# Performance work log

Measured on AMD Instinct MI355X. Metric: run time of the kernel, lower is better.

## Reference

```python
import jax, jax.numpy as jnp
import numpy as np

N = 100_000          # nodes
E = 600_000          # directed edges, stored in reverse pairs (2i <-> 2i+1)
D_NODE = 128
D_EDGE = 16
UNITS = 128
EDGE_STEPS = 4
NODE_STEPS = 4


def setup_inputs() -> dict:
    key = jax.random.key(0)
    ks = jax.random.split(key, 10)
    s = 0.05
    # undirected pairs -> both directions so every edge has a reverse edge
    u = jax.random.randint(ks[0], (E // 2,), 0, N, dtype=jnp.int32)
    v = jax.random.randint(ks[1], (E // 2,), 0, N, dtype=jnp.int32)
    edge_src = jnp.stack([u, v], axis=1).reshape(-1)  # [E]
    edge_dst = jnp.stack([v, u], axis=1).reshape(-1)  # [E]
    edge_rev = (jnp.arange(E, dtype=jnp.int32) ^ 1)   # reverse-edge index
    return dict(
        node_feature=jax.random.normal(ks[2], (N, D_NODE), jnp.float32),
        edge_feature=jax.random.normal(ks[3], (E, D_EDGE), jnp.float32),
        W_init=jax.random.normal(ks[4], (D_NODE + D_EDGE, UNITS), jnp.float32) * s,
        b_init=jnp.zeros((UNITS,), jnp.float32),
        W_edge=jax.random.normal(ks[5], (EDGE_STEPS, UNITS, UNITS), jnp.float32) * s,
        b_edge=jnp.zeros((EDGE_STEPS, UNITS), jnp.float32),
        W_gin0=jax.random.normal(ks[6], (D_NODE + UNITS, UNITS), jnp.float32) * s,
        W_gin=jax.random.normal(ks[7], (NODE_STEPS - 1, UNITS, UNITS), jnp.float32) * s,
        b_gin=jnp.zeros((NODE_STEPS, UNITS), jnp.float32),
        eps=jnp.zeros((NODE_STEPS,), jnp.float32),
        edge_src=edge_src,
        edge_dst=edge_dst,
        edge_rev=edge_rev,
    )


def reference(node_feature, edge_feature, W_init, b_init, W_edge, b_edge,
              W_gin0, W_gin, b_gin, eps, edge_src, edge_dst, edge_rev):
    relu = jax.nn.relu
    seg = lambda x: jax.ops.segment_sum(x, edge_dst, num_segments=N)

    # ---- EdgeConv stack (D-MPNN directed edge message passing) ----
    # initial edge state: act(W [x_src || e])
    h = relu(jnp.concatenate([node_feature[edge_src], edge_feature], axis=-1)
             @ W_init + b_init)                                  # [E, U]
    for t in range(EDGE_STEPS):
        agg = seg(h)                                             # [N, U] incoming sums
        m = agg[edge_src] - h[edge_rev]                          # exclude reverse edge
        h = relu(h + m @ W_edge[t] + b_edge[t])                  # residual edge update

    # ---- NodeReadout: sum incoming edge states per node ----
    readout = seg(h)                                             # [N, U]
    x = jnp.concatenate([node_feature, readout], axis=-1)        # [N, D_NODE + U]

    # ---- GINConv stack (use_edge_features=False) ----
    for t in range(NODE_STEPS):
        agg = seg(x[edge_src])                                   # [N, d] neighbor sum
        W = W_gin0 if t == 0 else W_gin[t - 1]
        x = relu(((1.0 + eps[t]) * x + agg) @ W + b_gin[t])      # [N, U]

    return x, h
```

## Files before the change

### kernel.cpp

```cpp
#include <hip/hip_runtime.h>

#define N_NODES 100000
#define N_EDGES 600000
#define SCAN_NB ((N_NODES + 255) / 256)

#define WOFF_I  0
#define WOFF_E  20480
#define WOFF_G0 86016
#define WOFF_G  118784
#define WTOTAL  167936
#define NFCONV_THREADS (N_NODES * 128 / 8)

typedef unsigned short u16;
typedef __attribute__((ext_vector_type(8))) short short8v;
typedef __attribute__((ext_vector_type(4))) short short4v;
typedef __attribute__((ext_vector_type(4))) float f32x4;
typedef __attribute__((ext_vector_type(2))) unsigned u32x2;
typedef __attribute__((ext_vector_type(8))) __bf16 bf16x8v;

__device__ __forceinline__ u16 f2bf(float f) {
  unsigned u = __builtin_bit_cast(unsigned, f);
  unsigned r = (u + 0x7fffu + ((u >> 16) & 1u)) >> 16;
  return (u16)r;
}
__device__ __forceinline__ float bf2f(u16 v) {
  unsigned u = ((unsigned)v) << 16;
  return __builtin_bit_cast(float, u);
}
__device__ __forceinline__ float bflo(unsigned u) {
  return __builtin_bit_cast(float, u << 16);
}
__device__ __forceinline__ float bfhi(unsigned u) {
  return __builtin_bit_cast(float, u & 0xffff0000u);
}
__device__ __forceinline__ short8v shfl_xor4_v(short8v v) {
  int4 iv = __builtin_bit_cast(int4, v);
  iv.x = __shfl_xor(iv.x, 4, 64);
  iv.y = __shfl_xor(iv.y, 4, 64);
  iv.z = __shfl_xor(iv.z, 4, 64);
  iv.w = __shfl_xor(iv.w, 4, 64);
  return __builtin_bit_cast(short8v, iv);
}

__global__ __launch_bounds__(256) void convert_all_kernel(const float* __restrict__ nf,
                                                          u16* __restrict__ nfro,
                                                          const float* __restrict__ Wi,
                                                          const float* __restrict__ We,
                                                          const float* __restrict__ Wg0,
                                                          const float* __restrict__ Wg,
                                                          u16* __restrict__ wout) {
  int tid = blockIdx.x * 256 + threadIdx.x;
  if (tid < NFCONV_THREADS) {
    size_t idx = (size_t)tid * 8;
    float4 a = *(const float4*)(nf + idx);
    float4 b = *(const float4*)(nf + idx + 4);
    short8v o = {(short)f2bf(a.x), (short)f2bf(a.y), (short)f2bf(a.z), (short)f2bf(a.w),
                 (short)f2bf(b.x), (short)f2bf(b.y), (short)f2bf(b.z), (short)f2bf(b.w)};
    size_t row = idx >> 7, col = idx & 127;
    *(short8v*)(nfro + row * 256 + col) = o;
    return;
  }
  int e = tid - NFCONV_THREADS;
  if (e >= WTOTAL) return;
  float v;
  if (e < WOFF_E) {
    int col = e / 160, k = e % 160;
    v = (k < 144) ? Wi[(size_t)k * 128 + col] : 0.f;
  } else if (e < WOFF_G0) {
    int r = e - WOFF_E;
    int m = r / 16384; r %= 16384;
    int col = r / 128, k = r % 128;
    v = We[(size_t)m * 16384 + (size_t)k * 128 + col];
  } else if (e < WOFF_G) {
    int r = e - WOFF_G0;
    int col = r / 256, k = r % 256;
    v = Wg0[(size_t)k * 128 + col];
  } else {
    int r = e - WOFF_G;
    int m = r / 16384; r %= 16384;
    int col = r / 128, k = r % 128;
    v = Wg[(size_t)m * 16384 + (size_t)k * 128 + col];
  }
  wout[e] = f2bf(v);
}

__global__ void hist_kernel(const int* __restrict__ dst, int* __restrict__ cnt) {
  int e = blockIdx.x * 256 + threadIdx.x;
  if (e < N_EDGES) atomicAdd(&cnt[dst[e]], 1);
}

__global__ __launch_bounds__(256) void scan1_kernel(int* __restrict__ cnt,
                                                    int* __restrict__ off,
                                                    int* __restrict__ blk) {
  __shared__ int s[256];
  int i = blockIdx.x * 256 + threadIdx.x;
  int v = (i < N_NODES) ? cnt[i] : 0;
  if (i < N_NODES) cnt[i] = 0;
  s[threadIdx.x] = v;
  __syncthreads();
  for (int d = 1; d < 256; d <<= 1) {
    int t = (threadIdx.x >= d) ? s[threadIdx.x - d] : 0;
    __syncthreads();
    s[threadIdx.x] += t;
    __syncthreads();
  }
  if (i < N_NODES) off[i] = s[threadIdx.x] - v;
  if (threadIdx.x == 255) blk[blockIdx.x] = s[255];
}

__global__ __launch_bounds__(512) void scan2_kernel(int* __restrict__ blk) {
  __shared__ int s[512];
  int v = (threadIdx.x < SCAN_NB) ? blk[threadIdx.x] : 0;
  s[threadIdx.x] = v;
  __syncthreads();
  for (int d = 1; d < 512; d <<= 1) {
    int t = (threadIdx.x >= d) ? s[threadIdx.x - d] : 0;
    __syncthreads();
    s[threadIdx.x] += t;
    __syncthreads();
  }
  if (threadIdx.x < SCAN_NB) blk[threadIdx.x] = s[threadIdx.x] - v;
}

__global__ __launch_bounds__(256) void scan3_kernel(int* __restrict__ off,
                                                    const int* __restrict__ blk) {
  int i = blockIdx.x * 256 + threadIdx.x;
  if (i < N_NODES) off[i] += blk[blockIdx.x];
  if (i == 0) off[N_NODES] = N_EDGES;
}

__global__ void fill_kernel(const int* __restrict__ dst, const int* __restrict__ src,
                            const int* __restrict__ off, int* __restrict__ cur,
                            int* __restrict__ csr_e, int* __restrict__ csr_s) {
  int e = blockIdx.x * 256 + threadIdx.x;
  if (e < N_EDGES) {
    int d = dst[e];
    int p = off[d] + atomicAdd(&cur[d], 1);
    csr_e[p] = e;
    csr_s[p] = src[e];
  }
}

__global__ __launch_bounds__(256) void segsum_hbf_kernel(const u16* __restrict__ hbf,
                                                         const int* __restrict__ off,
                                                         const int* __restrict__ csr_e,
                                                         u16* __restrict__ aggb) {
  int node = blockIdx.x * 8 + (threadIdx.x >> 5);
  int hl = threadIdx.x & 31;
  int p0 = off[node], p1 = off[node + 1];
  int deg = p1 - p0;
  int e_l = (hl < deg) ? csr_e[p0 + hl] : 0;
  float a0 = 0.f, a1 = 0.f, a2 = 0.f, a3 = 0.f;
  int jmax = min(deg, 32);
  for (int j = 0; j < jmax; ++j) {
    int e = __shfl(e_l, j, 32);
    u32x2 u = *(const u32x2*)(hbf + (size_t)e * 128 + 4 * hl);
    a0 += bflo(u.x); a1 += bfhi(u.x); a2 += bflo(u.y); a3 += bfhi(u.y);
  }
  for (int p = p0 + 32; p < p1; ++p) {
    int e = csr_e[p];
    u32x2 u = *(const u32x2*)(hbf + (size_t)e * 128 + 4 * hl);
    a0 += bflo(u.x); a1 += bfhi(u.x); a2 += bflo(u.y); a3 += bfhi(u.y);
  }
  u32x2 o = {(unsigned)f2bf(a0) | (((unsigned)f2bf(a1)) << 16),
             (unsigned)f2bf(a2) | (((unsigned)f2bf(a3)) << 16)};
  *(u32x2*)(aggb + (size_t)node * 128 + 4 * hl) = o;
}

__global__ __launch_bounds__(256) void segsum_readout_kernel(const u16* __restrict__ hbf,
                                                             const int* __restrict__ off,
                                                             const int* __restrict__ csr_e,
                                                             u16* __restrict__ ro) {
  int node = blockIdx.x * 8 + (threadIdx.x >> 5);
  int hl = threadIdx.x & 31;
  int p0 = off[node], p1 = off[node + 1];
  int deg = p1 - p0;
  int e_l = (hl < deg) ? csr_e[p0 + hl] : 0;
  float a0 = 0.f, a1 = 0.f, a2 = 0.f, a3 = 0.f;
  int jmax = min(deg, 32);
  for (int j = 0; j < jmax; ++j) {
    int e = __shfl(e_l, j, 32);
    u32x2 u = __builtin_nontemporal_load((const u32x2*)(hbf + (size_t)e * 128 + 4 * hl));
    a0 += bflo(u.x); a1 += bfhi(u.x); a2 += bflo(u.y); a3 += bfhi(u.y);
  }
  for (int p = p0 + 32; p < p1; ++p) {
    int e = csr_e[p];
    u32x2 u = __builtin_nontemporal_load((const u32x2*)(hbf + (size_t)e * 128 + 4 * hl));
    a0 += bflo(u.x); a1 += bfhi(u.x); a2 += bflo(u.y); a3 += bfhi(u.y);
  }
  u32x2 o = {(unsigned)f2bf(a0) | (((unsigned)f2bf(a1)) << 16),
             (unsigned)f2bf(a2) | (((unsigned)f2bf(a3)) << 16)};
  *(u32x2*)(ro + (size_t)node * 256 + 4 * hl) = o;
}

#define PREP_INIT 0
#define PREP_EDGE 1
#define PREP_GIN0 2
#define PREP_GINX 3
#define EPI_BR  1
#define EPI_ABR 2

template<int KSTEPS, int PREPM, int EPIM, int OUTBF, int TPB>
__global__ __launch_bounds__(256, (KSTEPS <= 5) ? 4 : 3) void mfma_gemm(
    const u16* __restrict__ Wt,
    const float* __restrict__ bias,
    const void* __restrict__ P0,
    const void* __restrict__ P1,
    const int* __restrict__ srcIdx,
    const int* __restrict__ csr_off,
    const int* __restrict__ csr_s,
    const float* __restrict__ epsp,
    float* __restrict__ OutF32,
    void* __restrict__ Out, int numRows) {
  constexpr int RS = KSTEPS * 32 + 8;
  constexpr bool WLATE = (KSTEPS >= 8);
  __shared__ short amem[64 * RS];
  const int t = threadIdx.x;
  const int l = t & 63;
  const int w = t >> 6;
  const int g = l >> 4;
  const int n0 = l & 15;

  short8v wf[KSTEPS][2];
  auto load_w = [&]() {
    #pragma unroll
    for (int s = 0; s < KSTEPS; ++s)
      #pragma unroll
      for (int ct = 0; ct < 2; ++ct)
        wf[s][ct] = *(const short8v*)(Wt + (size_t)((2 * w + ct) * 16 + n0) * (KSTEPS * 32) + 32 * s + 8 * g);
  };
  if constexpr (!WLATE) load_w();

  float bb[2];
  #pragma unroll
  for (int ct = 0; ct < 2; ++ct) bb[ct] = bias[(2 * w + ct) * 16 + n0];
  float alpha = 0.f;
  if constexpr (PREPM == PREP_GIN0 || PREPM == PREP_GINX) alpha = 1.f + epsp[0];

  for (int it = 0; it < TPB; ++it) {
    const int base = (blockIdx.x * TPB + it) * 64;
    short8v hself[4];

    if constexpr (PREPM == PREP_INIT) {
      const int i = t >> 2, q = t & 3;
      const int row = base + i;
      const int sn = srcIdx[row];
      const u16* nrow = (const u16*)P0 + (size_t)sn * 256 + q * 32;
      #pragma unroll
      for (int c = 0; c < 4; ++c)
        *(short8v*)(&amem[i * RS + q * 32 + 8 * c]) = *(const short8v*)(nrow + 8 * c);
      #pragma unroll
      for (int z = 0; z < 2; ++z) {
        int col = 128 + (2 * q + z) * 4;
        short4v o = {0, 0, 0, 0};
        if (col < 144) {
          f32x4 vv = __builtin_nontemporal_load(
              (const f32x4*)((const float*)P1 + (size_t)row * 16 + (col - 128)));
          o = {(short)f2bf(vv.x), (short)f2bf(vv.y), (short)f2bf(vv.z), (short)f2bf(vv.w)};
        }
        *(short4v*)(&amem[i * RS + col]) = o;
      }
    } else if constexpr (PREPM == PREP_EDGE) {
      const int i = t >> 2, q = t & 3;
      const int row = base + i;
      const int sn = srcIdx[row];
      const u16* arow = (const u16*)P0 + (size_t)sn * 128 + q * 32;
      const u16* hrow = (const u16*)P1 + (size_t)row * 128 + q * 32;
      short8v av[4];
      #pragma unroll
      for (int c = 0; c < 4; ++c) av[c] = *(const short8v*)(arow + 8 * c);
      #pragma unroll
      for (int c = 0; c < 4; ++c) hself[c] = *(const short8v*)(hrow + 8 * c);
      #pragma unroll
      for (int c = 0; c < 4; ++c) {
        short8v hrev = shfl_xor4_v(hself[c]);
        short8v o;
        #pragma unroll
        for (int j = 0; j < 8; ++j)
          o[j] = (short)f2bf(bf2f((u16)av[c][j]) - bf2f((u16)hrev[j]));
        *(short8v*)(&amem[i * RS + q * 32 + 8 * c]) = o;
      }
    } else if constexpr (PREPM == PREP_GIN0) {
      const int i2 = t >> 3, q = t & 7;
      #pragma unroll
      for (int half = 0; half < 2; ++half) {
        const int r = i2 + 32 * half;
        const int row = base + r;
        const int n = (row < numRows) ? row : (numRows - 1);
        const int p0 = csr_off[n], p1 = csr_off[n + 1];
        float acc[32];
        const u16* self = (const u16*)P0 + (size_t)n * 256 + 32 * q;
        #pragma unroll
        for (int c8 = 0; c8 < 4; ++c8) {
          short8v v = *(const short8v*)(self + 8 * c8);
          #pragma unroll
          for (int j = 0; j < 8; ++j) acc[8 * c8 + j] = alpha * bf2f((u16)v[j]);
        }
        for (int p = p0; p < p1; ++p) {
          const u16* nb = (const u16*)P0 + (size_t)csr_s[p] * 256 + 32 * q;
          #pragma unroll
          for (int c8 = 0; c8 < 4; ++c8) {
            short8v v = *(const short8v*)(nb + 8 * c8);
            #pragma unroll
            for (int j = 0; j < 8; ++j) acc[8 * c8 + j] += bf2f((u16)v[j]);
          }
        }
        #pragma unroll
        for (int c4 = 0; c4 < 8; ++c4) {
          short4v o = {(short)f2bf(acc[4 * c4 + 0]), (short)f2bf(acc[4 * c4 + 1]),
                       (short)f2bf(acc[4 * c4 + 2]), (short)f2bf(acc[4 * c4 + 3])};
          *(short4v*)(&amem[r * RS + 32 * q + 4 * c4]) = o;
        }
      }
    } else {
      const int i = t >> 2, q = t & 3;
      const int row = base + i;
      const int n = (row < numRows) ? row : (numRows - 1);
      const int p0 = csr_off[n], p1 = csr_off[n + 1];
      float acc[32];
      const u16* self = (const u16*)P0 + (size_t)n * 128 + 32 * q;
      #pragma unroll
      for (int c8 = 0; c8 < 4; ++c8) {
        short8v v = *(const short8v*)(self + 8 * c8);
        #pragma unroll
        for (int j = 0; j < 8; ++j) acc[8 * c8 + j] = alpha * bf2f((u16)v[j]);
      }
      for (int p = p0; p < p1; ++p) {
        const u16* nb = (const u16*)P0 + (size_t)csr_s[p] * 128 + 32 * q;
        #pragma unroll
        for (int c8 = 0; c8 < 4; ++c8) {
          short8v v = *(const short8v*)(nb + 8 * c8);
          #pragma unroll
          for (int j = 0; j < 8; ++j) acc[8 * c8 + j] += bf2f((u16)v[j]);
        }
      }
      #pragma unroll
      for (int c4 = 0; c4 < 8; ++c4) {
        short4v o = {(short)f2bf(acc[4 * c4 + 0]), (short)f2bf(acc[4 * c4 + 1]),
                     (short)f2bf(acc[4 * c4 + 2]), (short)f2bf(acc[4 * c4 + 3])};
        *(short4v*)(&amem[i * RS + 32 * q + 4 * c4]) = o;
      }
    }
    __syncthreads();
    if constexpr (WLATE) load_w();

    f32x4 acc[4][2];
    #pragma unroll
    for (int rt = 0; rt < 4; ++rt)
      #pragma unroll
      for (int ct = 0; ct < 2; ++ct) acc[rt][ct] = (f32x4){0.f, 0.f, 0.f, 0.f};
    #pragma unroll
    for (int s = 0; s < KSTEPS; ++s) {
      bf16x8v af[4];
      #pragma unroll
      for (int rt = 0; rt < 4; ++rt) {
        short8v araw = *(const short8v*)(&amem[(16 * rt + n0) * RS + s * 32 + g * 8]);
        af[rt] = __builtin_bit_cast(bf16x8v, araw);
      }
      #pragma unroll
      for (int rt = 0; rt < 4; ++rt)
        #pragma unroll
        for (int ct = 0; ct < 2; ++ct)
          acc[rt][ct] = __builtin_amdgcn_mfma_f32_16x16x32_bf16(
              af[rt], __builtin_bit_cast(bf16x8v, wf[s][ct]), acc[rt][ct], 0, 0, 0);
    }

    if constexpr (EPIM == EPI_ABR) {
      __syncthreads();
      {
        const int i = t >> 2, q = t & 3;
        #pragma unroll
        for (int c = 0; c < 4; ++c)
          *(short8v*)(&amem[i * RS + q * 32 + 8 * c]) = hself[c];
      }
      __syncthreads();
    }

    if constexpr (OUTBF) {
      if constexpr (EPIM != EPI_ABR) __syncthreads();
      #pragma unroll
      for (int rt = 0; rt < 4; ++rt) {
        #pragma unroll
        for (int ct = 0; ct < 2; ++ct) {
          #pragma unroll
          for (int r = 0; r < 4; ++r) {
            int lrow = 16 * rt + 4 * g + r;
            int lcol = (2 * w + ct) * 16 + n0;
            float o = acc[rt][ct][r];
            if constexpr (EPIM == EPI_ABR) o += bf2f((u16)amem[lrow * RS + lcol]);
            o = fmaxf(o + bb[ct], 0.f);
            if constexpr (OUTBF == 2)
              __builtin_nontemporal_store(o, &OutF32[(size_t)(base + lrow) * 128 + lcol]);
            amem[lrow * RS + lcol] = (short)f2bf(o);
          }
        }
      }
      __syncthreads();
      {
        const int i = t >> 2, q = t & 3;
        const int row = base + i;
        if (row < numRows) {
          u16* orow = (u16*)Out + (size_t)row * 128 + q * 32;
          #pragma unroll
          for (int c = 0; c < 4; ++c)
            *(short8v*)(orow + 8 * c) = *(const short8v*)(&amem[i * RS + q * 32 + 8 * c]);
        }
      }
    } else {
      #pragma unroll
      for (int rt = 0; rt < 4; ++rt) {
        #pragma unroll
        for (int ct = 0; ct < 2; ++ct) {
          #pragma unroll
          for (int r = 0; r < 4; ++r) {
            int row = base + 16 * rt + 4 * g + r;
            if (row < numRows) {
              int lcol = (2 * w + ct) * 16 + n0;
              float o = acc[rt][ct][r];
              o = fmaxf(o + bb[ct], 0.f);
              __builtin_nontemporal_store(o, &((float*)Out)[(size_t)row * 128 + lcol]);
            }
          }
        }
      }
    }
    __syncthreads();
  }
}

extern "C" void kernel_launch(void* const* d_in, const int* in_sizes, int n_in,
                              void* d_out, int out_size, void* d_ws, size_t ws_size,
                              hipStream_t stream) {
  const float* nf     = (const float*)d_in[0];
  const float* ef     = (const float*)d_in[1];
  const float* W_init = (const float*)d_in[2];
  const float* b_init = (const float*)d_in[3];
  const float* W_edge = (const float*)d_in[4];
  const float* b_edge = (const float*)d_in[5];
  const float* W_gin0 = (const float*)d_in[6];
  const float* W_gin  = (const float*)d_in[7];
  const float* b_gin  = (const float*)d_in[8];
  const float* eps    = (const float*)d_in[9];
  const int* esrc     = (const int*)d_in[10];
  const int* edst     = (const int*)d_in[11];

  float* xout  = (float*)d_out;
  float* h_out = xout + (size_t)N_NODES * 128;

  const size_t NB = (size_t)N_NODES * 128 * 2;
  const size_t EB = (size_t)N_EDGES * 128 * 2;
  char* wsb = (char*)d_ws;
  u16* aggbf   = (u16*)wsb;
  u16* xbf1    = (u16*)wsb;
  u16* hbf     = (u16*)(wsb + NB);
  u16* nfro    = (u16*)(wsb + NB + EB);
  u16* xbf0    = (u16*)(wsb + 3 * NB + EB);
  int* csr_off = (int*)(wsb + 4 * NB + EB);
  int* cursor  = csr_off + (N_NODES + 1);
  int* csr_e   = cursor + N_NODES;
  int* csr_s   = csr_e + N_EDGES;
  int* blk     = csr_s + N_EDGES;
  u16* wblob   = (u16*)(blk + SCAN_NB + 1);

  convert_all_kernel<<<(NFCONV_THREADS + WTOTAL + 255) / 256, 256, 0, stream>>>(
      nf, nfro, W_init, W_edge, W_gin0, W_gin, wblob);

  hipMemsetAsync(cursor, 0, N_NODES * sizeof(int), stream);
  hist_kernel<<<(N_EDGES + 255) / 256, 256, 0, stream>>>(edst, cursor);
  scan1_kernel<<<SCAN_NB, 256, 0, stream>>>(cursor, csr_off, blk);
  scan2_kernel<<<1, 512, 0, stream>>>(blk);
  scan3_kernel<<<SCAN_NB, 256, 0, stream>>>(csr_off, blk);
  fill_kernel<<<(N_EDGES + 255) / 256, 256, 0, stream>>>(edst, esrc, csr_off, cursor, csr_e, csr_s);

  const u16* wt_init = wblob + WOFF_I;
  const u16* wt_edge = wblob + WOFF_E;
  const u16* wt_gin0 = wblob + WOFF_G0;
  const u16* wt_gin  = wblob + WOFF_G;

  mfma_gemm<5, PREP_INIT, EPI_BR, 1, 5><<<1875, 256, 0, stream>>>(
      wt_init, b_init, nfro, ef, esrc, nullptr, nullptr, nullptr, nullptr, hbf, N_EDGES);

  for (int t = 0; t < 3; ++t) {
    segsum_hbf_kernel<<<N_NODES / 8, 256, 0, stream>>>(hbf, csr_off, csr_e, aggbf);
    mfma_gemm<4, PREP_EDGE, EPI_ABR, 1, 5><<<1875, 256, 0, stream>>>(
        wt_edge + (size_t)t * 16384, b_edge + (size_t)t * 128,
        aggbf, hbf, esrc, nullptr, nullptr, nullptr, nullptr, hbf, N_EDGES);
  }
  segsum_hbf_kernel<<<N_NODES / 8, 256, 0, stream>>>(hbf, csr_off, csr_e, aggbf);
  mfma_gemm<4, PREP_EDGE, EPI_ABR, 2, 5><<<1875, 256, 0, stream>>>(
      wt_edge + (size_t)3 * 16384, b_edge + (size_t)3 * 128,
      aggbf, hbf, esrc, nullptr, nullptr, nullptr, h_out, hbf, N_EDGES);

  segsum_readout_kernel<<<N_NODES / 8, 256, 0, stream>>>(hbf, csr_off, csr_e, nfro + 128);

  mfma_gemm<8, PREP_GIN0, EPI_BR, 1, 3><<<521, 256, 0, stream>>>(
      wt_gin0, b_gin, nfro, nullptr, nullptr, csr_off, csr_s, eps, nullptr, xbf0, N_NODES);

  mfma_gemm<4, PREP_GINX, EPI_BR, 1, 3><<<521, 256, 0, stream>>>(
      wt_gin, b_gin + 128, xbf0, nullptr, nullptr, csr_off, csr_s, eps + 1, nullptr, xbf1, N_NODES);
  mfma_gemm<4, PREP_GINX, EPI_BR, 1, 3><<<521, 256, 0, stream>>>(
      wt_gin + 16384, b_gin + 256, xbf1, nullptr, nullptr, csr_off, csr_s, eps + 2, nullptr, xbf0, N_NODES);
  mfma_gemm<4, PREP_GINX, EPI_BR, 0, 3><<<521, 256, 0, stream>>>(
      wt_gin + 2 * 16384, b_gin + 384, xbf0, nullptr, nullptr, csr_off, csr_s, eps + 3, nullptr, xout, N_NODES);

  (void)in_sizes; (void)n_in; (void)out_size; (void)ws_size;
}
```

Baseline: 1.031 ms.

## Widen segsum gathers to 16B, fuse histogram into convert, split GIN0 weight loads

The segment-sum kernels now use 16 lanes per node, each loading 16 bytes (8 bf16), instead of 32 lanes loading 8 bytes, so each node needs fewer, wider gather transactions and each block covers twice as many nodes. The destination-degree histogram is folded into the convert kernel as extra threads doing 8 atomics each, removing one kernel launch. The 8-K-step GEMM now loads its weight fragments in two halves of 4 steps, cutting register pressure so launch bounds can request 4 waves per SIMD for every instantiation. The risks are lower parallelism for nodes with many in-edges and the extra weight reloads in the split path.

Measured after the change: 1.030 ms. About the same (-0.0%).

```diff
diff --git a/kernel.cpp b/kernel.cpp
--- a/kernel.cpp
+++ b/kernel.cpp
@@ -10,12 +10,13 @@
 #define WOFF_G  118784
 #define WTOTAL  167936
 #define NFCONV_THREADS (N_NODES * 128 / 8)
+#define HIST_THREADS ((N_EDGES + 7) / 8)
 
 typedef unsigned short u16;
 typedef __attribute__((ext_vector_type(8))) short short8v;
 typedef __attribute__((ext_vector_type(4))) short short4v;
 typedef __attribute__((ext_vector_type(4))) float f32x4;
-typedef __attribute__((ext_vector_type(2))) unsigned u32x2;
+typedef __attribute__((ext_vector_type(4))) unsigned u32x4;
 typedef __attribute__((ext_vector_type(8))) __bf16 bf16x8v;
 
 __device__ __forceinline__ u16 f2bf(float f) {
@@ -48,7 +49,9 @@
                                                           const float* __restrict__ We,
                                                           const float* __restrict__ Wg0,
                                                           const float* __restrict__ Wg,
-                                                          u16* __restrict__ wout) {
+                                                          u16* __restrict__ wout,
+                                                          const int* __restrict__ dst,
+                                                          int* __restrict__ cnt) {
   int tid = blockIdx.x * 256 + threadIdx.x;
   if (tid < NFCONV_THREADS) {
     size_t idx = (size_t)tid * 8;
@@ -61,32 +64,35 @@
     return;
   }
   int e = tid - NFCONV_THREADS;
-  if (e >= WTOTAL) return;
-  float v;
-  if (e < WOFF_E) {
-    int col = e / 160, k = e % 160;
-    v = (k < 144) ? Wi[(size_t)k * 128 + col] : 0.f;
-  } else if (e < WOFF_G0) {
-    int r = e - WOFF_E;
-    int m = r / 16384; r %= 16384;
-    int col = r / 128, k = r % 128;
-    v = We[(size_t)m * 16384 + (size_t)k * 128 + col];
-  } else if (e < WOFF_G) {
-    int r = e - WOFF_G0;
-    int col = r / 256, k = r % 256;
-    v = Wg0[(size_t)k * 128 + col];
-  } else {
-    int r = e - WOFF_G;
-    int m = r / 16384; r %= 16384;
-    int col = r / 128, k = r % 128;
-    v = Wg[(size_t)m * 16384 + (size_t)k * 128 + col];
-  }
-  wout[e] = f2bf(v);
-}
-
-__global__ void hist_kernel(const int* __restrict__ dst, int* __restrict__ cnt) {
-  int e = blockIdx.x * 256 + threadIdx.x;
-  if (e < N_EDGES) atomicAdd(&cnt[dst[e]], 1);
+  if (e < WTOTAL) {
+    float v;
+    if (e < WOFF_E) {
+      int col = e / 160, k = e % 160;
+      v = (k < 144) ? Wi[(size_t)k * 128 + col] : 0.f;
+    } else if (e < WOFF_G0) {
+      int r = e - WOFF_E;
+      int m = r / 16384; r %= 16384;
+      int col = r / 128, k = r % 128;
+      v = We[(size_t)m * 16384 + (size_t)k * 128 + col];
+    } else if (e < WOFF_G) {
+      int r = e - WOFF_G0;
+      int col = r / 256, k = r % 256;
+      v = Wg0[(size_t)k * 128 + col];
+    } else {
+      int r = e - WOFF_G;
+      int m = r / 16384; r %= 16384;
+      int col = r / 128, k = r % 128;
+      v = Wg[(size_t)m * 16384 + (size_t)k * 128 + col];
+    }
+    wout[e] = f2bf(v);
+    return;
+  }
+  int hb = tid - NFCONV_THREADS - WTOTAL;
+  if (hb < HIST_THREADS) {
+    int e0 = hb * 8;
+    int e1 = min(e0 + 8, N_EDGES);
+    for (int ee = e0; ee < e1; ++ee) atomicAdd(&cnt[dst[ee]], 1);
+  }
 }
 
 __global__ __launch_bounds__(256) void scan1_kernel(int* __restrict__ cnt,
@@ -145,52 +151,60 @@
                                                          const int* __restrict__ off,
                                                          const int* __restrict__ csr_e,
                                                          u16* __restrict__ aggb) {
-  int node = blockIdx.x * 8 + (threadIdx.x >> 5);
-  int hl = threadIdx.x & 31;
+  int node = blockIdx.x * 16 + (threadIdx.x >> 4);
+  int hl = threadIdx.x & 15;
   int p0 = off[node], p1 = off[node + 1];
   int deg = p1 - p0;
   int e_l = (hl < deg) ? csr_e[p0 + hl] : 0;
-  float a0 = 0.f, a1 = 0.f, a2 = 0.f, a3 = 0.f;
-  int jmax = min(deg, 32);
+  float a0 = 0.f, a1 = 0.f, a2 = 0.f, a3 = 0.f, a4 = 0.f, a5 = 0.f, a6 = 0.f, a7 = 0.f;
+  int jmax = min(deg, 16);
   for (int j = 0; j < jmax; ++j) {
-    int e = __shfl(e_l, j, 32);
-    u32x2 u = *(const u32x2*)(hbf + (size_t)e * 128 + 4 * hl);
+    int e = __shfl(e_l, j, 16);
+    u32x4 u = *(const u32x4*)(hbf + (size_t)e * 128 + 8 * hl);
     a0 += bflo(u.x); a1 += bfhi(u.x); a2 += bflo(u.y); a3 += bfhi(u.y);
-  }
-  for (int p = p0 + 32; p < p1; ++p) {
+    a4 += bflo(u.z); a5 += bfhi(u.z); a6 += bflo(u.w); a7 += bfhi(u.w);
+  }
+  for (int p = p0 + 16; p < p1; ++p) {
     int e = csr_e[p];
-    u32x2 u = *(const u32x2*)(hbf + (size_t)e * 128 + 4 * hl);
+    u32x4 u = *(const u32x4*)(hbf + (size_t)e * 128 + 8 * hl);
     a0 += bflo(u.x); a1 += bfhi(u.x); a2 += bflo(u.y); a3 += bfhi(u.y);
-  }
-  u32x2 o = {(unsigned)f2bf(a0) | (((unsigned)f2bf(a1)) << 16),
-             (unsigned)f2bf(a2) | (((unsigned)f2bf(a3)) << 16)};
-  *(u32x2*)(aggb + (size_t)node * 128 + 4 * hl) = o;
+    a4 += bflo(u.z); a5 += bfhi(u.z); a6 += bflo(u.w); a7 += bfhi(u.w);
+  }
+  u32x4 o = {(unsigned)f2bf(a0) | (((unsigned)f2bf(a1)) << 16),
+             (unsigned)f2bf(a2) | (((unsigned)f2bf(a3)) << 16),
+             (unsigned)f2bf(a4) | (((unsigned)f2bf(a5)) << 16),
+             (unsigned)f2bf(a6) | (((unsigned)f2bf(a7)) << 16)};
+  *(u32x4*)(aggb + (size_t)node * 128 + 8 * hl) = o;
 }
 
 __global__ __launch_bounds__(256) void segsum_readout_kernel(const u16* __restrict__ hbf,
                                                              const int* __restrict__ off,
                                                              const int* __restrict__ csr_e,
                                                              u16* __restrict__ ro) {
-  int node = blockIdx.x * 8 + (threadIdx.x >> 5);
-  int hl = threadIdx.x & 31;
+  int node = blockIdx.x * 16 + (threadIdx.x >> 4);
+  int hl = threadIdx.x & 15;
   int p0 = off[node], p1 = off[node + 1];
   int deg = p1 - p0;
   int e_l = (hl < deg) ? csr_e[p0 + hl] : 0;
-  float a0 = 0.f, a1 = 0.f, a2 = 0.f, a3 = 0.f;
-  int jmax = min(deg, 32);
+  float a0 = 0.f, a1 = 0.f, a2 = 0.f, a3 = 0.f, a4 = 0.f, a5 = 0.f, a6 = 0.f, a7 = 0.f;
+  int jmax = min(deg, 16);
   for (int j = 0; j < jmax; ++j) {
-    int e = __shfl(e_l, j, 32);
-    u32x2 u = __builtin_nontemporal_load((const u32x2*)(hbf + (size_t)e * 128 + 4 * hl));
+    int e = __shfl(e_l, j, 16);
+    u32x4 u = __builtin_nontemporal_load((const u32x4*)(hbf + (size_t)e * 128 + 8 * hl));
     a0 += bflo(u.x); a1 += bfhi(u.x); a2 += bflo(u.y); a3 += bfhi(u.y);
-  }
-  for (int p = p0 + 32; p < p1; ++p) {
+    a4 += bflo(u.z); a5 += bfhi(u.z); a6 += bflo(u.w); a7 += bfhi(u.w);
+  }
+  for (int p = p0 + 16; p < p1; ++p) {
     int e = csr_e[p];
-    u32x2 u = __builtin_nontemporal_load((const u32x2*)(hbf + (size_t)e * 128 + 4 * hl));
+    u32x4 u = __builtin_nontemporal_load((const u32x4*)(hbf + (size_t)e * 128 + 8 * hl));
     a0 += bflo(u.x); a1 += bfhi(u.x); a2 += bflo(u.y); a3 += bfhi(u.y);
-  }
-  u32x2 o = {(unsigned)f2bf(a0) | (((unsigned)f2bf(a1)) << 16),
-             (unsigned)f2bf(a2) | (((unsigned)f2bf(a3)) << 16)};
-  *(u32x2*)(ro + (size_t)node * 256 + 4 * hl) = o;
+    a4 += bflo(u.z); a5 += bfhi(u.z); a6 += bflo(u.w); a7 += bfhi(u.w);
+  }
+  u32x4 o = {(unsigned)f2bf(a0) | (((unsigned)f2bf(a1)) << 16),
+             (unsigned)f2bf(a2) | (((unsigned)f2bf(a3)) << 16),
+             (unsigned)f2bf(a4) | (((unsigned)f2bf(a5)) << 16),
+             (unsigned)f2bf(a6) | (((unsigned)f2bf(a7)) << 16)};
+  *(u32x4*)(ro + (size_t)node * 256 + 8 * hl) = o;
 }
 
 #define PREP_INIT 0
@@ -201,7 +215,7 @@
 #define EPI_ABR 2
 
 template<int KSTEPS, int PREPM, int EPIM, int OUTBF, int TPB>
-__global__ __launch_bounds__(256, (KSTEPS <= 5) ? 4 : 3) void mfma_gemm(
+__global__ __launch_bounds__(256, 4) void mfma_gemm(
     const u16* __restrict__ Wt,
     const float* __restrict__ bias,
     const void* __restrict__ P0,
@@ -213,7 +227,8 @@
     float* __restrict__ OutF32,
     void* __restrict__ Out, int numRows) {
   constexpr int RS = KSTEPS * 32 + 8;
-  constexpr bool WLATE = (KSTEPS >= 8);
+  constexpr bool WSPLIT = (KSTEPS >= 8);
+  constexpr int WREG = WSPLIT ? 4 : KSTEPS;
   __shared__ short amem[64 * RS];
   const int t = threadIdx.x;
   const int l = t & 63;
@@ -221,15 +236,15 @@
   const int g = l >> 4;
   const int n0 = l & 15;
 
-  short8v wf[KSTEPS][2];
-  auto load_w = [&]() {
+  short8v wf[WREG][2];
+  auto load_w = [&](int sbase) {
     #pragma unroll
-    for (int s = 0; s < KSTEPS; ++s)
+    for (int s = 0; s < WREG; ++s)
       #pragma unroll
       for (int ct = 0; ct < 2; ++ct)
-        wf[s][ct] = *(const short8v*)(Wt + (size_t)((2 * w + ct) * 16 + n0) * (KSTEPS * 32) + 32 * s + 8 * g);
+        wf[s][ct] = *(const short8v*)(Wt + (size_t)((2 * w + ct) * 16 + n0) * (KSTEPS * 32) + 32 * (sbase + s) + 8 * g);
   };
-  if constexpr (!WLATE) load_w();
+  if constexpr (!WSPLIT) load_w(0);
 
   float bb[2];
   #pragma unroll
@@ -342,7 +357,6 @@
       }
     }
     __syncthreads();
-    if constexpr (WLATE) load_w();
 
     f32x4 acc[4][2];
     #pragma unroll
@@ -350,19 +364,24 @@
       #pragma unroll
       for (int ct = 0; ct < 2; ++ct) acc[rt][ct] = (f32x4){0.f, 0.f, 0.f, 0.f};
     #pragma unroll
-    for (int s = 0; s < KSTEPS; ++s) {
-      bf16x8v af[4];
-      #pragma unroll
-      for (int rt = 0; rt < 4; ++rt) {
-        short8v araw = *(const short8v*)(&amem[(16 * rt + n0) * RS + s * 32 + g * 8]);
-        af[rt] = __builtin_bit_cast(bf16x8v, araw);
-      }
-      #pragma unroll
-      for (int rt = 0; rt < 4; ++rt)
-        #pragma unroll
-        for (int ct = 0; ct < 2; ++ct)
-          acc[rt][ct] = __builtin_amdgcn_mfma_f32_16x16x32_bf16(
-              af[rt], __builtin_bit_cast(bf16x8v, wf[s][ct]), acc[rt][ct], 0, 0, 0);
+    for (int sb = 0; sb < (WSPLIT ? 2 : 1); ++sb) {
+      if constexpr (WSPLIT) load_w(sb * 4);
+      #pragma unroll
+      for (int s2 = 0; s2 < WREG; ++s2) {
+        const int s = sb * WREG + s2;
+        bf16x8v af[4];
+        #pragma unroll
+        for (int rt = 0; rt < 4; ++rt) {
+          short8v araw = *(const short8v*)(&amem[(16 * rt + n0) * RS + s * 32 + g * 8]);
+          af[rt] = __builtin_bit_cast(bf16x8v, araw);
+        }
+        #pragma unroll
+        for (int rt = 0; rt < 4; ++rt)
+          #pragma unroll
+          for (int ct = 0; ct < 2; ++ct)
+            acc[rt][ct] = __builtin_amdgcn_mfma_f32_16x16x32_bf16(
+                af[rt], __builtin_bit_cast(bf16x8v, wf[s2][ct]), acc[rt][ct], 0, 0, 0);
+      }
     }
 
     if constexpr (EPIM == EPI_ABR) {
@@ -462,11 +481,10 @@
   int* blk     = csr_s + N_EDGES;
   u16* wblob   = (u16*)(blk + SCAN_NB + 1);
 
-  convert_all_kernel<<<(NFCONV_THREADS + WTOTAL + 255) / 256, 256, 0, stream>>>(
-      nf, nfro, W_init, W_edge, W_gin0, W_gin, wblob);
-
   hipMemsetAsync(cursor, 0, N_NODES * sizeof(int), stream);
-  hist_kernel<<<(N_EDGES + 255) / 256, 256, 0, stream>>>(edst, cursor);
+  convert_all_kernel<<<(NFCONV_THREADS + WTOTAL + HIST_THREADS + 255) / 256, 256, 0, stream>>>(
+      nf, nfro, W_init, W_edge, W_gin0, W_gin, wblob, edst, cursor);
+
   scan1_kernel<<<SCAN_NB, 256, 0, stream>>>(cursor, csr_off, blk);
   scan2_kernel<<<1, 512, 0, stream>>>(blk);
   scan3_kernel<<<SCAN_NB, 256, 0, stream>>>(csr_off, blk);
@@ -481,17 +499,17 @@
       wt_init, b_init, nfro, ef, esrc, nullptr, nullptr, nullptr, nullptr, hbf, N_EDGES);
 
   for (int t = 0; t < 3; ++t) {
-    segsum_hbf_kernel<<<N_NODES / 8, 256, 0, stream>>>(hbf, csr_off, csr_e, aggbf);
+    segsum_hbf_kernel<<<N_NODES / 16, 256, 0, stream>>>(hbf, csr_off, csr_e, aggbf);
     mfma_gemm<4, PREP_EDGE, EPI_ABR, 1, 5><<<1875, 256, 0, stream>>>(
         wt_edge + (size_t)t * 16384, b_edge + (size_t)t * 128,
         aggbf, hbf, esrc, nullptr, nullptr, nullptr, nullptr, hbf, N_EDGES);
   }
-  segsum_hbf_kernel<<<N_NODES / 8, 256, 0, stream>>>(hbf, csr_off, csr_e, aggbf);
+  segsum_hbf_kernel<<<N_NODES / 16, 256, 0, stream>>>(hbf, csr_off, csr_e, aggbf);
   mfma_gemm<4, PREP_EDGE, EPI_ABR, 2, 5><<<1875, 256, 0, stream>>>(
       wt_edge + (size_t)3 * 16384, b_edge + (size_t)3 * 128,
       aggbf, hbf, esrc, nullptr, nullptr, nullptr, h_out, hbf, N_EDGES);
 
-  segsum_readout_kernel<<<N_NODES / 8, 256, 0, stream>>>(hbf, csr_off, csr_e, nfro + 128);
+  segsum_readout_kernel<<<N_NODES / 16, 256, 0, stream>>>(hbf, csr_off, csr_e, nfro + 128);
 
   mfma_gemm<8, PREP_GIN0, EPI_BR, 1, 3><<<521, 256, 0, stream>>>(
       wt_gin0, b_gin, nfro, nullptr, nullptr, csr_off, csr_s, eps, nullptr, xbf0, N_NODES);
```
